# Kernel optimization log

Measured on AMD Instinct MI355X. Metric: run time of the kernel, lower is better.

Reference implementation:

```python
import jax, jax.numpy as jnp
import numpy as np
import math

B, L, H, E = 4, 2048, 8, 64


def setup_inputs() -> dict:
    key = jax.random.key(0)
    kq, kk, kv, ks = jax.random.split(key, 4)
    return {
        "queries": jax.random.normal(kq, (B, L, H, E), dtype=jnp.float32),
        "keys": jax.random.normal(kk, (B, L, H, E), dtype=jnp.float32),
        "values": jax.random.normal(kv, (B, L, H, E), dtype=jnp.float32),
        "sigma": jax.random.normal(ks, (B, L, H), dtype=jnp.float32),
    }


def reference(queries, keys, values, sigma):
    Bq, Lq, Hq, Eq = queries.shape
    scale = 1.0 / math.sqrt(Eq)
    # QK^T: [B, H, L, S]
    scores = jnp.einsum("blhe,bshe->bhls", queries, keys)
    # triangular causal mask (mask_flag=True, attn_mask=None)
    causal = jnp.triu(jnp.ones((Lq, Lq), dtype=bool), k=1)
    scores = jnp.where(causal[None, None], -jnp.inf, scores)
    attn = scale * scores
    series = jax.nn.softmax(attn, axis=-1)  # dropout p=0.0 -> identity
    # sigma: [B, L, H] -> [B, H, L]
    sig = jnp.transpose(sigma, (0, 2, 1))
    sig = jax.nn.sigmoid(sig * 5.0) + 1e-5
    sig = jnp.power(3.0, sig) - 1.0
    sig = jnp.broadcast_to(sig[..., None], (Bq, Hq, Lq, Lq))  # [B,H,L,L]
    # |i - j| distances
    idx = jnp.arange(Lq, dtype=jnp.float32)
    dist = jnp.abs(idx[:, None] - idx[None, :])  # [L, L]
    prior = (1.0 / (math.sqrt(2.0 * math.pi) * sig)) * jnp.exp(
        -(dist[None, None] ** 2) / (2.0 * sig ** 2)
    )
    V = jnp.einsum("bhls,bshd->blhd", series, values)
    return V, series, prior, sig
```

## Files before the change

kernel.cpp:

```cpp
#include <hip/hip_runtime.h>
#include <math.h>

#define BB 4
#define LL 2048
#define HH 8
#define EE 64
#define TM 64
#define TN 64
#define SH 72

typedef _Float16 half4v __attribute__((ext_vector_type(4)));
typedef _Float16 half8v __attribute__((ext_vector_type(8)));
typedef float floatx4 __attribute__((ext_vector_type(4)));

static constexpr float SCALE = 0.125f;
static constexpr float LN3 = 1.0986122886681098f;
static constexpr float INV_SQRT_2PI = 0.3989422804014327f;
static constexpr size_t NMAT = (size_t)BB * HH * LL * LL;
static constexpr size_t SERIES_BASE = (size_t)BB * LL * HH * EE;
static constexpr size_t PRIOR_BASE = SERIES_BASE + NMAT;
static constexpr size_t SIG_BASE = PRIOR_BASE + NMAT;

__global__ __launch_bounds__(256, 2)
void anomaly_attn(const float* __restrict__ qg,
                  const float* __restrict__ kg,
                  const float* __restrict__ vg,
                  const float* __restrict__ sgg,
                  float* __restrict__ out) {
  __shared__ __attribute__((aligned(16))) _Float16 Qh[TM * SH];
  __shared__ __attribute__((aligned(16))) _Float16 Kh[TN * SH];
  __shared__ __attribute__((aligned(16))) _Float16 Vt[EE * SH];
  __shared__ __attribute__((aligned(16))) _Float16 Ph[TM * SH];
  __shared__ float s_sigv[TM], s_pinv[TM], s_c2[TM];

  const int t = threadIdx.x;
  const int lane = t & 63;
  const int w = t >> 6;
  const int quad = lane >> 4;
  const int l15 = lane & 15;
  const int bh = blockIdx.y;
  const int b = bh >> 3, h = bh & 7;
  const float4* q4 = (const float4*)qg;
  const float4* k4 = (const float4*)kg;
  const float4* v4 = (const float4*)vg;

  for (int half = 0; half < 2; ++half) {
    const int rt = half ? (31 - (int)blockIdx.x) : (int)blockIdx.x;
    const int i0 = rt * TM;
    const int nt = rt + 1;
    __syncthreads();

#pragma unroll
    for (int it = 0; it < 4; ++it) {
      int idx = t + 256 * it;
      int r = idx >> 4, c = idx & 15;
      float4 qv = q4[(((size_t)b * LL + i0 + r) * HH + h) * 16 + c];
      half4v hq = {(_Float16)qv.x, (_Float16)qv.y, (_Float16)qv.z, (_Float16)qv.w};
      *(half4v*)&Qh[r * SH + c * 4] = hq;
    }
    if (t < TM) {
      float sg = sgg[((size_t)b * LL + (i0 + t)) * HH + h];
      float sd = 1.0f / (1.0f + __expf(-5.0f * sg)) + 1e-5f;
      float sv = expm1f(sd * LN3);
      s_sigv[t] = sv;
      s_pinv[t] = INV_SQRT_2PI / sv;
      s_c2[t] = 0.5f / (sv * sv);
    }

    float lsum[4] = {0.f, 0.f, 0.f, 0.f};
    for (int jt = 0; jt < nt; ++jt) {
      const int j0 = jt * TN;
      __syncthreads();
#pragma unroll
      for (int it = 0; it < 4; ++it) {
        int idx = t + 256 * it;
        int r = idx >> 4, c = idx & 15;
        float4 kv = k4[(((size_t)b * LL + j0 + r) * HH + h) * 16 + c];
        half4v hk = {(_Float16)kv.x, (_Float16)kv.y, (_Float16)kv.z, (_Float16)kv.w};
        *(half4v*)&Kh[r * SH + c * 4] = hk;
      }
      __syncthreads();
      floatx4 acc[4] = {{0.f, 0.f, 0.f, 0.f}, {0.f, 0.f, 0.f, 0.f},
                        {0.f, 0.f, 0.f, 0.f}, {0.f, 0.f, 0.f, 0.f}};
#pragma unroll
      for (int ks = 0; ks < 2; ++ks) {
        half8v a = *(half8v*)&Qh[(w * 16 + l15) * SH + ks * 32 + quad * 8];
#pragma unroll
        for (int f = 0; f < 4; ++f) {
          half8v bf = *(half8v*)&Kh[(f * 16 + l15) * SH + ks * 32 + quad * 8];
          acc[f] = __builtin_amdgcn_mfma_f32_16x16x32_f16(a, bf, acc[f], 0, 0, 0);
        }
      }
#pragma unroll
      for (int f = 0; f < 4; ++f) {
        int j = j0 + f * 16 + l15;
#pragma unroll
        for (int r = 0; r < 4; ++r) {
          int i = i0 + w * 16 + quad * 4 + r;
          lsum[r] += (j <= i) ? __expf(acc[f][r] * SCALE) : 0.f;
        }
      }
    }
#pragma unroll
    for (int r = 0; r < 4; ++r) {
      lsum[r] += __shfl_xor(lsum[r], 1);
      lsum[r] += __shfl_xor(lsum[r], 2);
      lsum[r] += __shfl_xor(lsum[r], 4);
      lsum[r] += __shfl_xor(lsum[r], 8);
    }
    float linv[4];
#pragma unroll
    for (int r = 0; r < 4; ++r) linv[r] = 1.0f / lsum[r];

    floatx4 Oacc[4] = {{0.f, 0.f, 0.f, 0.f}, {0.f, 0.f, 0.f, 0.f},
                       {0.f, 0.f, 0.f, 0.f}, {0.f, 0.f, 0.f, 0.f}};
    for (int jt = 0; jt < nt; ++jt) {
      const int j0 = jt * TN;
      __syncthreads();
#pragma unroll
      for (int it = 0; it < 4; ++it) {
        int idx = t + 256 * it;
        int r = idx >> 4, c = idx & 15;
        float4 kv = k4[(((size_t)b * LL + j0 + r) * HH + h) * 16 + c];
        half4v hk = {(_Float16)kv.x, (_Float16)kv.y, (_Float16)kv.z, (_Float16)kv.w};
        *(half4v*)&Kh[r * SH + c * 4] = hk;
      }
      {
        const int tx = t & 15, ty = t >> 4;
        float4 vv[4];
#pragma unroll
        for (int rr = 0; rr < 4; ++rr)
          vv[rr] = v4[(((size_t)b * LL + j0 + ty * 4 + rr) * HH + h) * 16 + tx];
#pragma unroll
        for (int c = 0; c < 4; ++c) {
          half4v hv = {(_Float16)vv[0].x, (_Float16)vv[1].x, (_Float16)vv[2].x, (_Float16)vv[3].x};
          float e0 = c == 0 ? vv[0].x : c == 1 ? vv[0].y : c == 2 ? vv[0].z : vv[0].w;
          float e1 = c == 0 ? vv[1].x : c == 1 ? vv[1].y : c == 2 ? vv[1].z : vv[1].w;
          float e2 = c == 0 ? vv[2].x : c == 1 ? vv[2].y : c == 2 ? vv[2].z : vv[2].w;
          float e3 = c == 0 ? vv[3].x : c == 1 ? vv[3].y : c == 2 ? vv[3].z : vv[3].w;
          hv = (half4v){(_Float16)e0, (_Float16)e1, (_Float16)e2, (_Float16)e3};
          *(half4v*)&Vt[(tx * 4 + c) * SH + ty * 4] = hv;
        }
      }
      __syncthreads();
      floatx4 acc[4] = {{0.f, 0.f, 0.f, 0.f}, {0.f, 0.f, 0.f, 0.f},
                        {0.f, 0.f, 0.f, 0.f}, {0.f, 0.f, 0.f, 0.f}};
#pragma unroll
      for (int ks = 0; ks < 2; ++ks) {
        half8v a = *(half8v*)&Qh[(w * 16 + l15) * SH + ks * 32 + quad * 8];
#pragma unroll
        for (int f = 0; f < 4; ++f) {
          half8v bf = *(half8v*)&Kh[(f * 16 + l15) * SH + ks * 32 + quad * 8];
          acc[f] = __builtin_amdgcn_mfma_f32_16x16x32_f16(a, bf, acc[f], 0, 0, 0);
        }
      }
#pragma unroll
      for (int f = 0; f < 4; ++f) {
        int j = j0 + f * 16 + l15;
#pragma unroll
        for (int r = 0; r < 4; ++r) {
          int i = i0 + w * 16 + quad * 4 + r;
          float p = (j <= i) ? __expf(acc[f][r] * SCALE) * linv[r] : 0.f;
          Ph[(w * 16 + quad * 4 + r) * SH + f * 16 + l15] = (_Float16)p;
        }
      }
      __syncthreads();
#pragma unroll
      for (int rnd = 0; rnd < 2; ++rnd) {
        int idx = t + 256 * rnd;
        int r = idx >> 3, c8 = idx & 7;
        half8v p = *(half8v*)&Ph[r * SH + c8 * 8];
        float4 lo = {(float)p[0], (float)p[1], (float)p[2], (float)p[3]};
        float4 hi = {(float)p[4], (float)p[5], (float)p[6], (float)p[7]};
        size_t off = SERIES_BASE + ((size_t)bh * LL + i0 + r) * LL + j0 + c8 * 8;
        *(float4*)&out[off] = lo;
        *(float4*)&out[off + 4] = hi;
      }
#pragma unroll
      for (int ks = 0; ks < 2; ++ks) {
        half8v a = *(half8v*)&Ph[(w * 16 + l15) * SH + ks * 32 + quad * 8];
#pragma unroll
        for (int f = 0; f < 4; ++f) {
          half8v bv = *(half8v*)&Vt[(f * 16 + l15) * SH + ks * 32 + quad * 8];
          Oacc[f] = __builtin_amdgcn_mfma_f32_16x16x32_f16(a, bv, Oacc[f], 0, 0, 0);
        }
      }
    }
#pragma unroll
    for (int f = 0; f < 4; ++f) {
#pragma unroll
      for (int r = 0; r < 4; ++r) {
        int i = i0 + w * 16 + quad * 4 + r;
        out[(((size_t)b * LL + i) * HH + h) * EE + f * 16 + l15] = Oacc[f][r];
      }
    }
    for (int idx = t; idx < TM * 512; idx += 256) {
      int rr = idx >> 9, jq = idx & 511;
      float iv = s_pinv[rr], c2 = s_c2[rr], sv = s_sigv[rr];
      float fi = (float)(i0 + rr);
      float d0 = fi - (float)(jq * 4);
      float d1 = d0 - 1.0f, d2 = d0 - 2.0f, d3 = d0 - 3.0f;
      float4 pr;
      pr.x = iv * __expf(-d0 * d0 * c2);
      pr.y = iv * __expf(-d1 * d1 * c2);
      pr.z = iv * __expf(-d2 * d2 * c2);
      pr.w = iv * __expf(-d3 * d3 * c2);
      size_t off = ((size_t)bh * LL + (i0 + rr)) * LL + jq * 4;
      *(float4*)&out[PRIOR_BASE + off] = pr;
      float4 sg4 = {sv, sv, sv, sv};
      *(float4*)&out[SIG_BASE + off] = sg4;
    }
    {
      int jz = nt * TN;
      int nz4 = (LL - jz) >> 2;
      if (nz4 > 0) {
        float4 z = {0, 0, 0, 0};
        for (int rr = 0; rr < TM; ++rr) {
          float* rowp = &out[SERIES_BASE + ((size_t)bh * LL + (i0 + rr)) * LL + jz];
          for (int c = t; c < nz4; c += 256) {
            *(float4*)&rowp[c * 4] = z;
          }
        }
      }
    }
  }
}

extern "C" void kernel_launch(void* const* d_in, const int* in_sizes, int n_in,
                              void* d_out, int out_size, void* d_ws, size_t ws_size,
                              hipStream_t stream) {
  const float* q = (const float*)d_in[0];
  const float* k = (const float*)d_in[1];
  const float* v = (const float*)d_in[2];
  const float* sg = (const float*)d_in[3];
  float* out = (float*)d_out;
  dim3 grid(LL / TM / 2, BB * HH);
  anomaly_attn<<<grid, 256, 0, stream>>>(q, k, v, sg, out);
}
```

Measured before the change: 1.715 ms.

## Split prior/sigma/zero-fill writes into separate wide kernel with nontemporal stores

Moves the prior, broadcast sigma and upper-triangle zero writes out of the attention kernel into a standalone kernel launched with 2048 blocks, each wave handling whole rows. The attention kernel previously ran only 512 blocks, so these bandwidth-bound writes were spread over few CUs. The new kernel can saturate memory bandwidth across the whole GPU, and series stores now use nontemporal hints to avoid cache pollution. This adds one kernel launch and runs the fill serially before the attention kernel rather than overlapping with it.

Measured after the change: 1.763 ms. 1.03x slower.

```diff
diff --git a/kernel.cpp b/kernel.cpp
--- a/kernel.cpp
+++ b/kernel.cpp
@@ -21,17 +21,54 @@
 static constexpr size_t PRIOR_BASE = SERIES_BASE + NMAT;
 static constexpr size_t SIG_BASE = PRIOR_BASE + NMAT;
 
+__global__ __launch_bounds__(256, 8)
+void prior_sig_fill(const float* __restrict__ sgg, float* __restrict__ out) {
+  const int lane = threadIdx.x & 63;
+  const int wv = (blockIdx.x << 2) | (threadIdx.x >> 6);
+  const int nw = gridDim.x << 2;
+  const int totalRows = BB * HH * LL;
+  for (int row = wv; row < totalRows; row += nw) {
+    const int bh = row >> 11;
+    const int i = row & (LL - 1);
+    const int b = bh >> 3, h = bh & 7;
+    float sg = sgg[((size_t)b * LL + i) * HH + h];
+    float sd = 1.0f / (1.0f + __expf(-5.0f * sg)) + 1e-5f;
+    float sv = expm1f(sd * LN3);
+    float iv = INV_SQRT_2PI / sv;
+    float c2 = 0.5f / (sv * sv);
+    const size_t roff = ((size_t)bh * LL + i) * LL;
+    const floatx4 s4 = {sv, sv, sv, sv};
+    const float fi = (float)i;
+#pragma unroll
+    for (int it = 0; it < 8; ++it) {
+      int j = (it << 8) + (lane << 2);
+      float d0 = fi - (float)j;
+      float d1 = d0 - 1.0f, d2 = d0 - 2.0f, d3 = d0 - 3.0f;
+      floatx4 pr;
+      pr.x = iv * __expf(-d0 * d0 * c2);
+      pr.y = iv * __expf(-d1 * d1 * c2);
+      pr.z = iv * __expf(-d2 * d2 * c2);
+      pr.w = iv * __expf(-d3 * d3 * c2);
+      __builtin_nontemporal_store(pr, (floatx4*)&out[PRIOR_BASE + roff + j]);
+      __builtin_nontemporal_store(s4, (floatx4*)&out[SIG_BASE + roff + j]);
+    }
+    const int jz = ((i >> 6) + 1) << 6;
+    const floatx4 z = {0.f, 0.f, 0.f, 0.f};
+    for (int j = jz + (lane << 2); j < LL; j += 256) {
+      __builtin_nontemporal_store(z, (floatx4*)&out[SERIES_BASE + roff + j]);
+    }
+  }
+}
+
 __global__ __launch_bounds__(256, 2)
 void anomaly_attn(const float* __restrict__ qg,
                   const float* __restrict__ kg,
                   const float* __restrict__ vg,
-                  const float* __restrict__ sgg,
                   float* __restrict__ out) {
   __shared__ __attribute__((aligned(16))) _Float16 Qh[TM * SH];
   __shared__ __attribute__((aligned(16))) _Float16 Kh[TN * SH];
   __shared__ __attribute__((aligned(16))) _Float16 Vt[EE * SH];
   __shared__ __attribute__((aligned(16))) _Float16 Ph[TM * SH];
-  __shared__ float s_sigv[TM], s_pinv[TM], s_c2[TM];
 
   const int t = threadIdx.x;
   const int lane = t & 63;
@@ -58,14 +95,6 @@
       half4v hq = {(_Float16)qv.x, (_Float16)qv.y, (_Float16)qv.z, (_Float16)qv.w};
       *(half4v*)&Qh[r * SH + c * 4] = hq;
     }
-    if (t < TM) {
-      float sg = sgg[((size_t)b * LL + (i0 + t)) * HH + h];
-      float sd = 1.0f / (1.0f + __expf(-5.0f * sg)) + 1e-5f;
-      float sv = expm1f(sd * LN3);
-      s_sigv[t] = sv;
-      s_pinv[t] = INV_SQRT_2PI / sv;
-      s_c2[t] = 0.5f / (sv * sv);
-    }
 
     float lsum[4] = {0.f, 0.f, 0.f, 0.f};
     for (int jt = 0; jt < nt; ++jt) {
@@ -133,12 +162,11 @@
           vv[rr] = v4[(((size_t)b * LL + j0 + ty * 4 + rr) * HH + h) * 16 + tx];
 #pragma unroll
         for (int c = 0; c < 4; ++c) {
-          half4v hv = {(_Float16)vv[0].x, (_Float16)vv[1].x, (_Float16)vv[2].x, (_Float16)vv[3].x};
           float e0 = c == 0 ? vv[0].x : c == 1 ? vv[0].y : c == 2 ? vv[0].z : vv[0].w;
           float e1 = c == 0 ? vv[1].x : c == 1 ? vv[1].y : c == 2 ? vv[1].z : vv[1].w;
           float e2 = c == 0 ? vv[2].x : c == 1 ? vv[2].y : c == 2 ? vv[2].z : vv[2].w;
           float e3 = c == 0 ? vv[3].x : c == 1 ? vv[3].y : c == 2 ? vv[3].z : vv[3].w;
-          hv = (half4v){(_Float16)e0, (_Float16)e1, (_Float16)e2, (_Float16)e3};
+          half4v hv = {(_Float16)e0, (_Float16)e1, (_Float16)e2, (_Float16)e3};
           *(half4v*)&Vt[(tx * 4 + c) * SH + ty * 4] = hv;
         }
       }
@@ -170,11 +198,11 @@
         int idx = t + 256 * rnd;
         int r = idx >> 3, c8 = idx & 7;
         half8v p = *(half8v*)&Ph[r * SH + c8 * 8];
-        float4 lo = {(float)p[0], (float)p[1], (float)p[2], (float)p[3]};
-        float4 hi = {(float)p[4], (float)p[5], (float)p[6], (float)p[7]};
+        floatx4 lo = {(float)p[0], (float)p[1], (float)p[2], (float)p[3]};
+        floatx4 hi = {(float)p[4], (float)p[5], (float)p[6], (float)p[7]};
         size_t off = SERIES_BASE + ((size_t)bh * LL + i0 + r) * LL + j0 + c8 * 8;
-        *(float4*)&out[off] = lo;
-        *(float4*)&out[off + 4] = hi;
+        __builtin_nontemporal_store(lo, (floatx4*)&out[off]);
+        __builtin_nontemporal_store(hi, (floatx4*)&out[off + 4]);
       }
 #pragma unroll
       for (int ks = 0; ks < 2; ++ks) {
@@ -192,35 +220,6 @@
       for (int r = 0; r < 4; ++r) {
         int i = i0 + w * 16 + quad * 4 + r;
         out[(((size_t)b * LL + i) * HH + h) * EE + f * 16 + l15] = Oacc[f][r];
-      }
-    }
-    for (int idx = t; idx < TM * 512; idx += 256) {
-      int rr = idx >> 9, jq = idx & 511;
-      float iv = s_pinv[rr], c2 = s_c2[rr], sv = s_sigv[rr];
-      float fi = (float)(i0 + rr);
-      float d0 = fi - (float)(jq * 4);
-      float d1 = d0 - 1.0f, d2 = d0 - 2.0f, d3 = d0 - 3.0f;
-      float4 pr;
-      pr.x = iv * __expf(-d0 * d0 * c2);
-      pr.y = iv * __expf(-d1 * d1 * c2);
-      pr.z = iv * __expf(-d2 * d2 * c2);
-      pr.w = iv * __expf(-d3 * d3 * c2);
-      size_t off = ((size_t)bh * LL + (i0 + rr)) * LL + jq * 4;
-      *(float4*)&out[PRIOR_BASE + off] = pr;
-      float4 sg4 = {sv, sv, sv, sv};
-      *(float4*)&out[SIG_BASE + off] = sg4;
-    }
-    {
-      int jz = nt * TN;
-      int nz4 = (LL - jz) >> 2;
-      if (nz4 > 0) {
-        float4 z = {0, 0, 0, 0};
-        for (int rr = 0; rr < TM; ++rr) {
-          float* rowp = &out[SERIES_BASE + ((size_t)bh * LL + (i0 + rr)) * LL + jz];
-          for (int c = t; c < nz4; c += 256) {
-            *(float4*)&rowp[c * 4] = z;
-          }
-        }
       }
     }
   }
@@ -234,6 +233,7 @@
   const float* v = (const float*)d_in[2];
   const float* sg = (const float*)d_in[3];
   float* out = (float*)d_out;
+  prior_sig_fill<<<dim3(2048), 256, 0, stream>>>(sg, out);
   dim3 grid(LL / TM / 2, BB * HH);
-  anomaly_attn<<<grid, 256, 0, stream>>>(q, k, v, sg, out);
+  anomaly_attn<<<grid, 256, 0, stream>>>(q, k, v, out);
 }
```

## Double key tile to 128 with 512 threads and use nontemporal output stores

Applied to the files above, without the earlier changes.

The key/value tile grows from 64 to 128 columns and the block goes from 4 to 8 waves. Each wave pair splits the tile's columns for QK^T, and the two partial row sums are combined through shared memory before normalisation. The P·V product is split across waves by output feature instead of by row group. Each wave now writes its own slice of the series tile straight from its own Ph region, which removes one block barrier per tile. All series, prior, sigma and zero-fill writes switch to nontemporal stores to reduce cache pollution on this write-heavy kernel. The trade-off is extra masked work in the last tile when the row-tile count is odd, plus higher register and LDS pressure per block.

Result: slower. 1.769 ms (+3.2%).

```diff
diff --git a/kernel.cpp b/kernel.cpp
--- a/kernel.cpp
+++ b/kernel.cpp
@@ -6,8 +6,9 @@
 #define HH 8
 #define EE 64
 #define TM 64
-#define TN 64
+#define TN 128
 #define SH 72
+#define SH2 136
 
 typedef _Float16 half4v __attribute__((ext_vector_type(4)));
 typedef _Float16 half8v __attribute__((ext_vector_type(8)));
@@ -21,7 +22,7 @@
 static constexpr size_t PRIOR_BASE = SERIES_BASE + NMAT;
 static constexpr size_t SIG_BASE = PRIOR_BASE + NMAT;
 
-__global__ __launch_bounds__(256, 2)
+__global__ __launch_bounds__(512, 4)
 void anomaly_attn(const float* __restrict__ qg,
                   const float* __restrict__ kg,
                   const float* __restrict__ vg,
@@ -29,13 +30,16 @@
                   float* __restrict__ out) {
   __shared__ __attribute__((aligned(16))) _Float16 Qh[TM * SH];
   __shared__ __attribute__((aligned(16))) _Float16 Kh[TN * SH];
-  __shared__ __attribute__((aligned(16))) _Float16 Vt[EE * SH];
-  __shared__ __attribute__((aligned(16))) _Float16 Ph[TM * SH];
+  __shared__ __attribute__((aligned(16))) _Float16 Vt[EE * SH2];
+  __shared__ __attribute__((aligned(16))) _Float16 Ph[TM * SH2];
+  __shared__ float s_red[2][TM];
   __shared__ float s_sigv[TM], s_pinv[TM], s_c2[TM];
 
   const int t = threadIdx.x;
   const int lane = t & 63;
   const int w = t >> 6;
+  const int rg = w & 3;
+  const int jh = w >> 2;
   const int quad = lane >> 4;
   const int l15 = lane & 15;
   const int bh = blockIdx.y;
@@ -47,12 +51,13 @@
   for (int half = 0; half < 2; ++half) {
     const int rt = half ? (31 - (int)blockIdx.x) : (int)blockIdx.x;
     const int i0 = rt * TM;
-    const int nt = rt + 1;
+    const int nt64 = rt + 1;
+    const int nt = (nt64 + 1) >> 1;
     __syncthreads();
 
 #pragma unroll
-    for (int it = 0; it < 4; ++it) {
-      int idx = t + 256 * it;
+    for (int it = 0; it < 2; ++it) {
+      int idx = t + 512 * it;
       int r = idx >> 4, c = idx & 15;
       float4 qv = q4[(((size_t)b * LL + i0 + r) * HH + h) * 16 + c];
       half4v hq = {(_Float16)qv.x, (_Float16)qv.y, (_Float16)qv.z, (_Float16)qv.w};
@@ -73,7 +78,7 @@
       __syncthreads();
 #pragma unroll
       for (int it = 0; it < 4; ++it) {
-        int idx = t + 256 * it;
+        int idx = t + 512 * it;
         int r = idx >> 4, c = idx & 15;
         float4 kv = k4[(((size_t)b * LL + j0 + r) * HH + h) * 16 + c];
         half4v hk = {(_Float16)kv.x, (_Float16)kv.y, (_Float16)kv.z, (_Float16)kv.w};
@@ -84,19 +89,19 @@
                         {0.f, 0.f, 0.f, 0.f}, {0.f, 0.f, 0.f, 0.f}};
 #pragma unroll
       for (int ks = 0; ks < 2; ++ks) {
-        half8v a = *(half8v*)&Qh[(w * 16 + l15) * SH + ks * 32 + quad * 8];
+        half8v a = *(half8v*)&Qh[(rg * 16 + l15) * SH + ks * 32 + quad * 8];
 #pragma unroll
         for (int f = 0; f < 4; ++f) {
-          half8v bf = *(half8v*)&Kh[(f * 16 + l15) * SH + ks * 32 + quad * 8];
+          half8v bf = *(half8v*)&Kh[(jh * 64 + f * 16 + l15) * SH + ks * 32 + quad * 8];
           acc[f] = __builtin_amdgcn_mfma_f32_16x16x32_f16(a, bf, acc[f], 0, 0, 0);
         }
       }
 #pragma unroll
       for (int f = 0; f < 4; ++f) {
-        int j = j0 + f * 16 + l15;
+        int j = j0 + jh * 64 + f * 16 + l15;
 #pragma unroll
         for (int r = 0; r < 4; ++r) {
-          int i = i0 + w * 16 + quad * 4 + r;
+          int i = i0 + rg * 16 + quad * 4 + r;
           lsum[r] += (j <= i) ? __expf(acc[f][r] * SCALE) : 0.f;
         }
       }
@@ -108,18 +113,25 @@
       lsum[r] += __shfl_xor(lsum[r], 4);
       lsum[r] += __shfl_xor(lsum[r], 8);
     }
+    if (l15 == 0) {
+#pragma unroll
+      for (int r = 0; r < 4; ++r) s_red[jh][rg * 16 + quad * 4 + r] = lsum[r];
+    }
+    __syncthreads();
     float linv[4];
 #pragma unroll
-    for (int r = 0; r < 4; ++r) linv[r] = 1.0f / lsum[r];
-
-    floatx4 Oacc[4] = {{0.f, 0.f, 0.f, 0.f}, {0.f, 0.f, 0.f, 0.f},
-                       {0.f, 0.f, 0.f, 0.f}, {0.f, 0.f, 0.f, 0.f}};
+    for (int r = 0; r < 4; ++r) {
+      int row = rg * 16 + quad * 4 + r;
+      linv[r] = 1.0f / (s_red[0][row] + s_red[1][row]);
+    }
+
+    floatx4 Oacc[2] = {{0.f, 0.f, 0.f, 0.f}, {0.f, 0.f, 0.f, 0.f}};
     for (int jt = 0; jt < nt; ++jt) {
       const int j0 = jt * TN;
       __syncthreads();
 #pragma unroll
       for (int it = 0; it < 4; ++it) {
-        int idx = t + 256 * it;
+        int idx = t + 512 * it;
         int r = idx >> 4, c = idx & 15;
         float4 kv = k4[(((size_t)b * LL + j0 + r) * HH + h) * 16 + c];
         half4v hk = {(_Float16)kv.x, (_Float16)kv.y, (_Float16)kv.z, (_Float16)kv.w};
@@ -133,13 +145,12 @@
           vv[rr] = v4[(((size_t)b * LL + j0 + ty * 4 + rr) * HH + h) * 16 + tx];
 #pragma unroll
         for (int c = 0; c < 4; ++c) {
-          half4v hv = {(_Float16)vv[0].x, (_Float16)vv[1].x, (_Float16)vv[2].x, (_Float16)vv[3].x};
           float e0 = c == 0 ? vv[0].x : c == 1 ? vv[0].y : c == 2 ? vv[0].z : vv[0].w;
           float e1 = c == 0 ? vv[1].x : c == 1 ? vv[1].y : c == 2 ? vv[1].z : vv[1].w;
           float e2 = c == 0 ? vv[2].x : c == 1 ? vv[2].y : c == 2 ? vv[2].z : vv[2].w;
           float e3 = c == 0 ? vv[3].x : c == 1 ? vv[3].y : c == 2 ? vv[3].z : vv[3].w;
-          hv = (half4v){(_Float16)e0, (_Float16)e1, (_Float16)e2, (_Float16)e3};
-          *(half4v*)&Vt[(tx * 4 + c) * SH + ty * 4] = hv;
+          half4v hv = {(_Float16)e0, (_Float16)e1, (_Float16)e2, (_Float16)e3};
+          *(half4v*)&Vt[(tx * 4 + c) * SH2 + ty * 4] = hv;
         }
       }
       __syncthreads();
@@ -147,78 +158,79 @@
                         {0.f, 0.f, 0.f, 0.f}, {0.f, 0.f, 0.f, 0.f}};
 #pragma unroll
       for (int ks = 0; ks < 2; ++ks) {
-        half8v a = *(half8v*)&Qh[(w * 16 + l15) * SH + ks * 32 + quad * 8];
+        half8v a = *(half8v*)&Qh[(rg * 16 + l15) * SH + ks * 32 + quad * 8];
 #pragma unroll
         for (int f = 0; f < 4; ++f) {
-          half8v bf = *(half8v*)&Kh[(f * 16 + l15) * SH + ks * 32 + quad * 8];
+          half8v bf = *(half8v*)&Kh[(jh * 64 + f * 16 + l15) * SH + ks * 32 + quad * 8];
           acc[f] = __builtin_amdgcn_mfma_f32_16x16x32_f16(a, bf, acc[f], 0, 0, 0);
         }
       }
 #pragma unroll
       for (int f = 0; f < 4; ++f) {
-        int j = j0 + f * 16 + l15;
+        int j = j0 + jh * 64 + f * 16 + l15;
 #pragma unroll
         for (int r = 0; r < 4; ++r) {
-          int i = i0 + w * 16 + quad * 4 + r;
+          int i = i0 + rg * 16 + quad * 4 + r;
           float p = (j <= i) ? __expf(acc[f][r] * SCALE) * linv[r] : 0.f;
-          Ph[(w * 16 + quad * 4 + r) * SH + f * 16 + l15] = (_Float16)p;
-        }
-      }
-      __syncthreads();
+          Ph[(rg * 16 + quad * 4 + r) * SH2 + jh * 64 + f * 16 + l15] = (_Float16)p;
+        }
+      }
 #pragma unroll
       for (int rnd = 0; rnd < 2; ++rnd) {
-        int idx = t + 256 * rnd;
-        int r = idx >> 3, c8 = idx & 7;
-        half8v p = *(half8v*)&Ph[r * SH + c8 * 8];
-        float4 lo = {(float)p[0], (float)p[1], (float)p[2], (float)p[3]};
-        float4 hi = {(float)p[4], (float)p[5], (float)p[6], (float)p[7]};
-        size_t off = SERIES_BASE + ((size_t)bh * LL + i0 + r) * LL + j0 + c8 * 8;
-        *(float4*)&out[off] = lo;
-        *(float4*)&out[off + 4] = hi;
-      }
-#pragma unroll
-      for (int ks = 0; ks < 2; ++ks) {
-        half8v a = *(half8v*)&Ph[(w * 16 + l15) * SH + ks * 32 + quad * 8];
-#pragma unroll
-        for (int f = 0; f < 4; ++f) {
-          half8v bv = *(half8v*)&Vt[(f * 16 + l15) * SH + ks * 32 + quad * 8];
-          Oacc[f] = __builtin_amdgcn_mfma_f32_16x16x32_f16(a, bv, Oacc[f], 0, 0, 0);
-        }
-      }
-    }
-#pragma unroll
-    for (int f = 0; f < 4; ++f) {
+        int row = rg * 16 + rnd * 8 + (lane >> 3);
+        int c8 = lane & 7;
+        half8v p = *(half8v*)&Ph[row * SH2 + jh * 64 + c8 * 8];
+        floatx4 lo = {(float)p[0], (float)p[1], (float)p[2], (float)p[3]};
+        floatx4 hi = {(float)p[4], (float)p[5], (float)p[6], (float)p[7]};
+        size_t off = SERIES_BASE + ((size_t)bh * LL + i0 + row) * LL + j0 + jh * 64 + c8 * 8;
+        __builtin_nontemporal_store(lo, (floatx4*)&out[off]);
+        __builtin_nontemporal_store(hi, (floatx4*)&out[off + 4]);
+      }
+      __syncthreads();
+#pragma unroll
+      for (int ks = 0; ks < 4; ++ks) {
+        half8v a = *(half8v*)&Ph[(rg * 16 + l15) * SH2 + ks * 32 + quad * 8];
+#pragma unroll
+        for (int f2 = 0; f2 < 2; ++f2) {
+          half8v bv = *(half8v*)&Vt[(jh * 32 + f2 * 16 + l15) * SH2 + ks * 32 + quad * 8];
+          Oacc[f2] = __builtin_amdgcn_mfma_f32_16x16x32_f16(a, bv, Oacc[f2], 0, 0, 0);
+        }
+      }
+    }
+#pragma unroll
+    for (int f2 = 0; f2 < 2; ++f2) {
 #pragma unroll
       for (int r = 0; r < 4; ++r) {
-        int i = i0 + w * 16 + quad * 4 + r;
-        out[(((size_t)b * LL + i) * HH + h) * EE + f * 16 + l15] = Oacc[f][r];
-      }
-    }
-    for (int idx = t; idx < TM * 512; idx += 256) {
+        int i = i0 + rg * 16 + quad * 4 + r;
+        int e = jh * 32 + f2 * 16 + l15;
+        out[(((size_t)b * LL + i) * HH + h) * EE + e] = Oacc[f2][r];
+      }
+    }
+    for (int idx = t; idx < TM * 512; idx += 512) {
       int rr = idx >> 9, jq = idx & 511;
       float iv = s_pinv[rr], c2 = s_c2[rr], sv = s_sigv[rr];
       float fi = (float)(i0 + rr);
       float d0 = fi - (float)(jq * 4);
       float d1 = d0 - 1.0f, d2 = d0 - 2.0f, d3 = d0 - 3.0f;
-      float4 pr;
+      floatx4 pr;
       pr.x = iv * __expf(-d0 * d0 * c2);
       pr.y = iv * __expf(-d1 * d1 * c2);
       pr.z = iv * __expf(-d2 * d2 * c2);
       pr.w = iv * __expf(-d3 * d3 * c2);
       size_t off = ((size_t)bh * LL + (i0 + rr)) * LL + jq * 4;
-      *(float4*)&out[PRIOR_BASE + off] = pr;
-      float4 sg4 = {sv, sv, sv, sv};
-      *(float4*)&out[SIG_BASE + off] = sg4;
+      __builtin_nontemporal_store(pr, (floatx4*)&out[PRIOR_BASE + off]);
+      floatx4 sg4 = {sv, sv, sv, sv};
+      __builtin_nontemporal_store(sg4, (floatx4*)&out[SIG_BASE + off]);
     }
     {
       int jz = nt * TN;
       int nz4 = (LL - jz) >> 2;
       if (nz4 > 0) {
-        float4 z = {0, 0, 0, 0};
+        const floatx4 z = {0.f, 0.f, 0.f, 0.f};
         for (int rr = 0; rr < TM; ++rr) {
           float* rowp = &out[SERIES_BASE + ((size_t)bh * LL + (i0 + rr)) * LL + jz];
-          for (int c = t; c < nz4; c += 256) {
-            *(float4*)&rowp[c * 4] = z;
+          for (int c = t; c < nz4; c += 512) {
+            __builtin_nontemporal_store(z, (floatx4*)&rowp[c * 4]);
           }
         }
       }
@@ -235,5 +247,5 @@
   const float* sg = (const float*)d_in[3];
   float* out = (float*)d_out;
   dim3 grid(LL / TM / 2, BB * HH);
-  anomaly_attn<<<grid, 256, 0, stream>>>(q, k, v, sg, out);
+  anomaly_attn<<<grid, 512, 0, stream>>>(q, k, v, sg, out);
 }
```

## Double row tile to 128 with 512-thread blocks and split K/V loading

Applied to the files above, without the earlier changes.

Doubles the query-row tile to 128 rows and the block to 512 threads (8 waves), so each K/V tile loaded from global memory is shared by twice as many rows. In the second pass, half of the threads load and transpose V while the other half load K, instead of every thread doing both. Each wave now writes out its own series rows, which removes one block-wide barrier per tile. In exchange the grid shrinks to 256 blocks, which may reduce occupancy and load balance, and the 512-thread launch bound may raise register pressure.

New measurement: 1.750 ms. 1.02x slower.

```diff
diff --git a/kernel.cpp b/kernel.cpp
--- a/kernel.cpp
+++ b/kernel.cpp
@@ -5,7 +5,7 @@
 #define LL 2048
 #define HH 8
 #define EE 64
-#define TM 64
+#define TM 128
 #define TN 64
 #define SH 72
 
@@ -21,7 +21,7 @@
 static constexpr size_t PRIOR_BASE = SERIES_BASE + NMAT;
 static constexpr size_t SIG_BASE = PRIOR_BASE + NMAT;
 
-__global__ __launch_bounds__(256, 2)
+__global__ __launch_bounds__(512, 2)
 void anomaly_attn(const float* __restrict__ qg,
                   const float* __restrict__ kg,
                   const float* __restrict__ vg,
@@ -45,14 +45,14 @@
   const float4* v4 = (const float4*)vg;
 
   for (int half = 0; half < 2; ++half) {
-    const int rt = half ? (31 - (int)blockIdx.x) : (int)blockIdx.x;
+    const int rt = half ? (15 - (int)blockIdx.x) : (int)blockIdx.x;
     const int i0 = rt * TM;
-    const int nt = rt + 1;
+    const int nt = 2 * rt + 2;
     __syncthreads();
 
 #pragma unroll
     for (int it = 0; it < 4; ++it) {
-      int idx = t + 256 * it;
+      int idx = t + 512 * it;
       int r = idx >> 4, c = idx & 15;
       float4 qv = q4[(((size_t)b * LL + i0 + r) * HH + h) * 16 + c];
       half4v hq = {(_Float16)qv.x, (_Float16)qv.y, (_Float16)qv.z, (_Float16)qv.w};
@@ -72,8 +72,8 @@
       const int j0 = jt * TN;
       __syncthreads();
 #pragma unroll
-      for (int it = 0; it < 4; ++it) {
-        int idx = t + 256 * it;
+      for (int it = 0; it < 2; ++it) {
+        int idx = t + 512 * it;
         int r = idx >> 4, c = idx & 15;
         float4 kv = k4[(((size_t)b * LL + j0 + r) * HH + h) * 16 + c];
         half4v hk = {(_Float16)kv.x, (_Float16)kv.y, (_Float16)kv.z, (_Float16)kv.w};
@@ -117,15 +117,7 @@
     for (int jt = 0; jt < nt; ++jt) {
       const int j0 = jt * TN;
       __syncthreads();
-#pragma unroll
-      for (int it = 0; it < 4; ++it) {
-        int idx = t + 256 * it;
-        int r = idx >> 4, c = idx & 15;
-        float4 kv = k4[(((size_t)b * LL + j0 + r) * HH + h) * 16 + c];
-        half4v hk = {(_Float16)kv.x, (_Float16)kv.y, (_Float16)kv.z, (_Float16)kv.w};
-        *(half4v*)&Kh[r * SH + c * 4] = hk;
-      }
-      {
+      if (t < 256) {
         const int tx = t & 15, ty = t >> 4;
         float4 vv[4];
 #pragma unroll
@@ -133,13 +125,22 @@
           vv[rr] = v4[(((size_t)b * LL + j0 + ty * 4 + rr) * HH + h) * 16 + tx];
 #pragma unroll
         for (int c = 0; c < 4; ++c) {
-          half4v hv = {(_Float16)vv[0].x, (_Float16)vv[1].x, (_Float16)vv[2].x, (_Float16)vv[3].x};
           float e0 = c == 0 ? vv[0].x : c == 1 ? vv[0].y : c == 2 ? vv[0].z : vv[0].w;
           float e1 = c == 0 ? vv[1].x : c == 1 ? vv[1].y : c == 2 ? vv[1].z : vv[1].w;
           float e2 = c == 0 ? vv[2].x : c == 1 ? vv[2].y : c == 2 ? vv[2].z : vv[2].w;
           float e3 = c == 0 ? vv[3].x : c == 1 ? vv[3].y : c == 2 ? vv[3].z : vv[3].w;
-          hv = (half4v){(_Float16)e0, (_Float16)e1, (_Float16)e2, (_Float16)e3};
+          half4v hv = {(_Float16)e0, (_Float16)e1, (_Float16)e2, (_Float16)e3};
           *(half4v*)&Vt[(tx * 4 + c) * SH + ty * 4] = hv;
+        }
+      } else {
+        const int tk = t - 256;
+#pragma unroll
+        for (int it = 0; it < 4; ++it) {
+          int idx = tk + 256 * it;
+          int r = idx >> 4, c = idx & 15;
+          float4 kv = k4[(((size_t)b * LL + j0 + r) * HH + h) * 16 + c];
+          half4v hk = {(_Float16)kv.x, (_Float16)kv.y, (_Float16)kv.z, (_Float16)kv.w};
+          *(half4v*)&Kh[r * SH + c * 4] = hk;
         }
       }
       __syncthreads();
@@ -164,18 +165,18 @@
           Ph[(w * 16 + quad * 4 + r) * SH + f * 16 + l15] = (_Float16)p;
         }
       }
-      __syncthreads();
 #pragma unroll
       for (int rnd = 0; rnd < 2; ++rnd) {
-        int idx = t + 256 * rnd;
-        int r = idx >> 3, c8 = idx & 7;
-        half8v p = *(half8v*)&Ph[r * SH + c8 * 8];
-        float4 lo = {(float)p[0], (float)p[1], (float)p[2], (float)p[3]};
-        float4 hi = {(float)p[4], (float)p[5], (float)p[6], (float)p[7]};
-        size_t off = SERIES_BASE + ((size_t)bh * LL + i0 + r) * LL + j0 + c8 * 8;
-        *(float4*)&out[off] = lo;
-        *(float4*)&out[off + 4] = hi;
-      }
+        int row = w * 16 + rnd * 8 + (lane >> 3);
+        int c8 = lane & 7;
+        half8v p = *(half8v*)&Ph[row * SH + c8 * 8];
+        floatx4 lo = {(float)p[0], (float)p[1], (float)p[2], (float)p[3]};
+        floatx4 hi = {(float)p[4], (float)p[5], (float)p[6], (float)p[7]};
+        size_t off = SERIES_BASE + ((size_t)bh * LL + i0 + row) * LL + j0 + c8 * 8;
+        *(floatx4*)&out[off] = lo;
+        *(floatx4*)&out[off + 4] = hi;
+      }
+      __syncthreads();
 #pragma unroll
       for (int ks = 0; ks < 2; ++ks) {
         half8v a = *(half8v*)&Ph[(w * 16 + l15) * SH + ks * 32 + quad * 8];
@@ -194,31 +195,31 @@
         out[(((size_t)b * LL + i) * HH + h) * EE + f * 16 + l15] = Oacc[f][r];
       }
     }
-    for (int idx = t; idx < TM * 512; idx += 256) {
+    for (int idx = t; idx < TM * 512; idx += 512) {
       int rr = idx >> 9, jq = idx & 511;
       float iv = s_pinv[rr], c2 = s_c2[rr], sv = s_sigv[rr];
       float fi = (float)(i0 + rr);
       float d0 = fi - (float)(jq * 4);
       float d1 = d0 - 1.0f, d2 = d0 - 2.0f, d3 = d0 - 3.0f;
-      float4 pr;
+      floatx4 pr;
       pr.x = iv * __expf(-d0 * d0 * c2);
       pr.y = iv * __expf(-d1 * d1 * c2);
       pr.z = iv * __expf(-d2 * d2 * c2);
       pr.w = iv * __expf(-d3 * d3 * c2);
       size_t off = ((size_t)bh * LL + (i0 + rr)) * LL + jq * 4;
-      *(float4*)&out[PRIOR_BASE + off] = pr;
-      float4 sg4 = {sv, sv, sv, sv};
-      *(float4*)&out[SIG_BASE + off] = sg4;
+      *(floatx4*)&out[PRIOR_BASE + off] = pr;
+      floatx4 sg4 = {sv, sv, sv, sv};
+      *(floatx4*)&out[SIG_BASE + off] = sg4;
     }
     {
       int jz = nt * TN;
       int nz4 = (LL - jz) >> 2;
       if (nz4 > 0) {
-        float4 z = {0, 0, 0, 0};
+        const floatx4 z = {0.f, 0.f, 0.f, 0.f};
         for (int rr = 0; rr < TM; ++rr) {
           float* rowp = &out[SERIES_BASE + ((size_t)bh * LL + (i0 + rr)) * LL + jz];
-          for (int c = t; c < nz4; c += 256) {
-            *(float4*)&rowp[c * 4] = z;
+          for (int c = t; c < nz4; c += 512) {
+            *(floatx4*)&rowp[c * 4] = z;
           }
         }
       }
@@ -234,6 +235,6 @@
   const float* v = (const float*)d_in[2];
   const float* sg = (const float*)d_in[3];
   float* out = (float*)d_out;
-  dim3 grid(LL / TM / 2, BB * HH);
-  anomaly_attn<<<grid, 256, 0, stream>>>(q, k, v, sg, out);
+  dim3 grid(16 / 2, BB * HH);
+  anomaly_attn<<<grid, 512, 0, stream>>>(q, k, v, sg, out);
 }
```
